# Optimization experiments

Measured on AMD Instinct MI355X. Metric: run time of the kernel, lower is better.

Reference implementation:

```python
import jax, jax.numpy as jnp
import numpy as np

EMBED_DIM = 768
HEADS = 8
HEAD_DIM = 128  # gnn_hidden_dim
OUT_DIM = HEADS * HEAD_DIM  # 1024, concat=True
NEG_SLOPE = 0.2  # PyG GATConv leaky_relu slope


def setup_inputs() -> dict:
    key = jax.random.key(0)
    ks = jax.random.split(key, 12)
    N, E = 10000, 160000
    x = jax.random.normal(ks[0], (N, EMBED_DIM), dtype=jnp.float32)
    edge_index = jax.random.randint(ks[1], (2, E), 0, N, dtype=jnp.int32)
    edge_attr = jax.random.uniform(ks[2], (E, 1), dtype=jnp.float32)
    # GATConv params (single layer, edge_dim=1)
    sc = 1.0 / np.sqrt(EMBED_DIM)
    W = jax.random.normal(ks[3], (EMBED_DIM, OUT_DIM), dtype=jnp.float32) * sc
    att_src = jax.random.normal(ks[4], (HEADS, HEAD_DIM), dtype=jnp.float32) * 0.1
    att_dst = jax.random.normal(ks[5], (HEADS, HEAD_DIM), dtype=jnp.float32) * 0.1
    W_edge = jax.random.normal(ks[6], (1, OUT_DIM), dtype=jnp.float32)
    att_edge = jax.random.normal(ks[7], (HEADS, HEAD_DIM), dtype=jnp.float32) * 0.1
    bias = jnp.zeros((OUT_DIM,), dtype=jnp.float32)
    # final classifier: in = 3*OUT_DIM (global pool + text node + image node)
    clf_W = jax.random.normal(ks[8], (3 * OUT_DIM, 2), dtype=jnp.float32) * (1.0 / np.sqrt(3 * OUT_DIM))
    clf_b = jnp.zeros((2,), dtype=jnp.float32)
    return {
        'x': x, 'edge_index': edge_index, 'edge_attr': edge_attr,
        'text_idx': 0, 'image_idx': 1,
        'W': W, 'att_src': att_src, 'att_dst': att_dst,
        'W_edge': W_edge, 'att_edge': att_edge, 'bias': bias,
        'clf_W': clf_W, 'clf_b': clf_b,
    }


def gat_layer(x, edge_index, edge_attr, W, att_src, att_dst, W_edge, att_edge, bias):
    N = x.shape[0]
    # add self-loops with edge_attr = mean of existing edge_attr (PyG default fill_value='mean')
    loop = jnp.arange(N, dtype=edge_index.dtype)
    ei = jnp.concatenate([edge_index, jnp.stack([loop, loop])], axis=1)
    ea_mean = jnp.mean(edge_attr, axis=0, keepdims=True)
    ea = jnp.concatenate([edge_attr, jnp.broadcast_to(ea_mean, (N, edge_attr.shape[1]))], axis=0)
    src, dst = ei[0], ei[1]
    xs = (x @ W).reshape(N, HEADS, HEAD_DIM)             # [N, H, C]
    a_src = jnp.einsum('nhc,hc->nh', xs, att_src)        # per-node src logits
    a_dst = jnp.einsum('nhc,hc->nh', xs, att_dst)
    e_emb = (ea @ W_edge).reshape(-1, HEADS, HEAD_DIM)   # [Etot, H, C]
    a_edge = jnp.einsum('ehc,hc->eh', e_emb, att_edge)
    alpha = jax.nn.leaky_relu(a_src[src] + a_dst[dst] + a_edge, NEG_SLOPE)  # [Etot, H]
    # softmax over incoming edges of each dst node
    m = jax.ops.segment_max(alpha, dst, num_segments=N)
    ex = jnp.exp(alpha - m[dst])
    denom = jax.ops.segment_sum(ex, dst, num_segments=N)
    w = ex / denom[dst]                                  # normalized attention [Etot, H]
    msg = xs[src] * w[:, :, None]                        # [Etot, H, C]
    out = jax.ops.segment_sum(msg, dst, num_segments=N)  # [N, H, C]
    return out.reshape(N, OUT_DIM) + bias


def reference(x, edge_index, edge_attr, text_idx, image_idx,
              W, att_src, att_dst, W_edge, att_edge, bias, clf_W, clf_b):
    # single GAT layer (num_gat_layers=1 -> no ELU/dropout after, eval mode)
    h = gat_layer(x, edge_index, edge_attr, W, att_src, att_dst, W_edge, att_edge, bias)
    g = jnp.mean(h, axis=0, keepdims=True)               # global_mean_pool, batch=None
    t = h[text_idx][None, :]
    im = h[image_idx][None, :]
    fused = jnp.concatenate([g, t, im], axis=1)          # [1, 3*OUT_DIM]
    logits = fused @ clf_W + clf_b                       # [1, 2]
    return logits
```

## Files before the change

### kernel.cpp

```cpp
#include <hip/hip_runtime.h>

#define NN 10000
#define EE 160000
#define ETOT (EE + NN)
#define EMB 768
#define ODIM 1024
#define NEG 0.2f
#define CAP 56

#define OFF_P      0
#define OFF_Q      12288
#define OFF_EAP    12296
#define OFF_EAACC  12360
#define OFF_CNTD   12364
#define OFF_CNTS   22364
#define ZERO_START 12364
#define ZERO_CNT   20000
#define OFF_A      32368
#define OFF_SAED   192368
#define OFF_DAES   1312368
#define OFF_RDEN   2432368
#define OFF_G      2512368

#define SELF_MARK 3.0e38f

__global__ __launch_bounds__(256) void k1f(
    const float* __restrict__ W, const float* __restrict__ att_src,
    const float* __restrict__ att_dst, const float* __restrict__ W_edge,
    const float* __restrict__ att_edge, const float* __restrict__ edge_attr,
    const float* __restrict__ bias, const float* __restrict__ clf_W,
    const float* __restrict__ clf_b, float* __restrict__ out,
    const int* __restrict__ ei, float* __restrict__ ws) {
  __shared__ float sred[8];
  int b = blockIdx.x;
  if (b < 48) {
    int tid = b * 256 + threadIdx.x;
    int k = tid >> 4, j = tid & 15, h = j & 7;
    const float* att = (j < 8) ? att_src : att_dst;
    const float4* wp = (const float4*)(W + k * ODIM + h * 128);
    const float4* ap = (const float4*)(att + h * 128);
    float acc = 0.f;
    #pragma unroll 8
    for (int c = 0; c < 32; ++c) {
      float4 w4 = wp[c], a4 = ap[c];
      acc += w4.x * a4.x + w4.y * a4.y + w4.z * a4.z + w4.w * a4.w;
    }
    ws[OFF_P + tid] = acc;
  } else if (b == 48) {
    if (threadIdx.x < 8) {
      int h = threadIdx.x;
      float acc = 0.f;
      #pragma unroll 8
      for (int c = 0; c < 128; ++c) acc += W_edge[h * 128 + c] * att_edge[h * 128 + c];
      ws[OFF_Q + h] = acc;
    }
  } else if (b == 49) {
    int t = threadIdx.x;
    float b0 = 0.f, b1 = 0.f;
    for (int i = t; i < 3072; i += 256) {
      float f = bias[i & 1023];
      b0 += f * clf_W[2 * i];
      b1 += f * clf_W[2 * i + 1];
    }
    #pragma unroll
    for (int o = 32; o > 0; o >>= 1) {
      b0 += __shfl_down(b0, o, 64);
      b1 += __shfl_down(b1, o, 64);
    }
    if ((t & 63) == 0) { sred[(t >> 6) * 2] = b0; sred[(t >> 6) * 2 + 1] = b1; }
    __syncthreads();
    if (t == 0) {
      out[0] = clf_b[0] + sred[0] + sred[2] + sred[4] + sred[6];
      out[1] = clf_b[1] + sred[1] + sred[3] + sred[5] + sred[7];
    }
  } else if (b < 74) {
    int t = (b - 50) * 256 + threadIdx.x;
    int k = t >> 3, h = t & 7;
    const float4* wseg = (const float4*)(W + k * ODIM + h * 128);
    float acc[6] = {0.f, 0.f, 0.f, 0.f, 0.f, 0.f};
    for (int c4 = 0; c4 < 32; ++c4) {
      float4 wv = wseg[c4];
      #pragma unroll
      for (int d = 0; d < 3; ++d) {
        const float4* cp = (const float4*)(clf_W + 2 * (1024 * d + h * 128 + c4 * 4));
        float4 q0 = cp[0], q1 = cp[1];
        acc[d * 2 + 0] += wv.x * q0.x + wv.y * q0.z + wv.z * q1.x + wv.w * q1.z;
        acc[d * 2 + 1] += wv.x * q0.y + wv.y * q0.w + wv.z * q1.y + wv.w * q1.w;
      }
    }
    #pragma unroll
    for (int d = 0; d < 3; ++d) {
      ws[OFF_G + d * 12288 + k * 16 + h * 2 + 0] = acc[d * 2 + 0];
      ws[OFF_G + d * 12288 + k * 16 + h * 2 + 1] = acc[d * 2 + 1];
    }
  } else if (b < 138) {
    int bi = b - 74;
    float acc = 0.f;
    for (int i = bi * 256 + threadIdx.x; i < EE; i += 64 * 256) acc += edge_attr[i];
    #pragma unroll
    for (int off = 32; off > 0; off >>= 1) acc += __shfl_down(acc, off, 64);
    if ((threadIdx.x & 63) == 0) sred[threadIdx.x >> 6] = acc;
    __syncthreads();
    if (threadIdx.x == 0)
      ws[OFF_EAP + bi] = sred[0] + sred[1] + sred[2] + sred[3];
  } else {
    int e = (b - 138) * 256 + threadIdx.x;
    if (e >= ETOT) return;
    int src, dst; float ea;
    if (e < EE) { src = ei[e]; dst = ei[EE + e]; ea = edge_attr[e]; }
    else { src = dst = e - EE; ea = SELF_MARK; }
    int* cntd = (int*)(ws + OFF_CNTD);
    int* cnts = (int*)(ws + OFF_CNTS);
    int pd = atomicAdd(&cntd[dst], 1);
    if (pd < CAP) {
      float2 pr; pr.x = __int_as_float(src); pr.y = ea;
      ((float2*)(ws + OFF_SAED))[dst * CAP + pd] = pr;
    }
    int ps = atomicAdd(&cnts[src], 1);
    if (ps < CAP) {
      float2 pr; pr.x = __int_as_float(dst); pr.y = ea;
      ((float2*)(ws + OFF_DAES))[src * CAP + ps] = pr;
    }
  }
}

__global__ __launch_bounds__(256) void kAx(const float* __restrict__ x,
                                           float* __restrict__ ws) {
  __shared__ float smem[12288];
  if (blockIdx.x == 313) {
    if (threadIdx.x < 64) {
      float v = ws[OFF_EAP + threadIdx.x];
      #pragma unroll
      for (int o = 32; o > 0; o >>= 1) v += __shfl_down(v, o, 64);
      if (threadIdx.x == 0) ws[OFF_EAACC] = v;
    }
    return;
  }
  for (int i = threadIdx.x; i < 3072; i += 256)
    ((float4*)smem)[i] = ((const float4*)(ws + OFF_P))[i];
  __syncthreads();
  int nl = threadIdx.x & 31, cg = threadIdx.x >> 5;
  int n = blockIdx.x * 32 + nl;
  float a[16];
  #pragma unroll
  for (int j = 0; j < 16; ++j) a[j] = 0.f;
  if (n < NN) {
    const float4* xr = (const float4*)(x + n * EMB + cg * 96);
    for (int kk = 0; kk < 24; ++kk) {
      float4 xv = xr[kk];
      const float* pr = &smem[(cg * 96 + kk * 4) * 16];
      #pragma unroll
      for (int j = 0; j < 16; ++j) a[j] += xv.x * pr[j];
      #pragma unroll
      for (int j = 0; j < 16; ++j) a[j] += xv.y * pr[16 + j];
      #pragma unroll
      for (int j = 0; j < 16; ++j) a[j] += xv.z * pr[32 + j];
      #pragma unroll
      for (int j = 0; j < 16; ++j) a[j] += xv.w * pr[48 + j];
    }
  }
  __syncthreads();
  #pragma unroll
  for (int j = 0; j < 16; ++j) smem[(cg * 16 + j) * 33 + nl] = a[j];
  __syncthreads();
  for (int w = threadIdx.x; w < 512; w += 256) {
    int rnl = w >> 4, j = w & 15;
    int nn = blockIdx.x * 32 + rnl;
    if (nn < NN) {
      float s = 0.f;
      #pragma unroll
      for (int c2 = 0; c2 < 8; ++c2) s += smem[(c2 * 16 + j) * 33 + rnl];
      ws[OFF_A + nn * 16 + j] = s;
    }
  }
}

__global__ __launch_bounds__(128) void kD(float* __restrict__ ws) {
  int t = blockIdx.x * 128 + threadIdx.x;
  int dst = t >> 3, h = t & 7;
  int deg = ((const int*)(ws + OFF_CNTD))[dst];
  if (deg > CAP) deg = CAP;
  float adh = ws[OFF_A + dst * 16 + 8 + h];
  float qh = ws[OFF_Q + h];
  float mean = ws[OFF_EAACC] * (1.0f / EE);
  const float2* prow = (const float2*)(ws + OFF_SAED) + dst * CAP;
  float den = 0.f;
  #pragma unroll 4
  for (int j = 0; j < deg; ++j) {
    float2 pr = prow[j];
    int srcj = __float_as_int(pr.x);
    float ae = pr.y;
    if (ae > 1e37f) ae = mean;
    float v = ws[OFF_A + srcj * 16 + h] + adh + ae * qh;
    v = (v >= 0.f) ? v : NEG * v;
    den += __expf(v);
  }
  ws[OFF_RDEN + t] = 1.0f / den;
}

__global__ __launch_bounds__(256, 3) void kF(const float* __restrict__ x,
                                             const int* __restrict__ tptr,
                                             const int* __restrict__ iptr,
                                             float* __restrict__ out,
                                             float* __restrict__ ws) {
  __shared__ float smem[12864];
  int t = threadIdx.x;
  float mean = ws[OFF_EAACC] * (1.0f / EE);
  float c0 = 0.f, c1 = 0.f;
  float scale;
  if (blockIdx.x < 625) {
    scale = 1.0f / NN;
    int base = blockIdx.x * 16;
    if (t >= 128) {
      for (int i = t - 128; i < 3072; i += 128)
        ((float4*)smem)[i] = ((const float4*)(ws + OFF_G))[i];
    } else {
      int nl = t >> 3, h = t & 7;
      int n = base + nl;
      int deg = ((const int*)(ws + OFF_CNTS))[n];
      if (deg > CAP) deg = CAP;
      float ash = ws[OFF_A + n * 16 + h];
      float qh = ws[OFF_Q + h];
      const float2* prow = (const float2*)(ws + OFF_DAES) + n * CAP;
      float s = 0.f;
      #pragma unroll 4
      for (int j = 0; j < deg; ++j) {
        float2 pr = prow[j];
        int dd = __float_as_int(pr.x);
        float ae = pr.y;
        if (ae > 1e37f) ae = mean;
        float v = ash + ws[OFF_A + dd * 16 + 8 + h] + ae * qh;
        v = (v >= 0.f) ? v : NEG * v;
        s += __expf(v) * ws[OFF_RDEN + dd * 8 + h];
      }
      smem[12288 + nl * 8 + h] = s;
    }
    __syncthreads();
    int nl = t & 15, cgp = t >> 4;
    int n = base + nl;
    float a[16];
    #pragma unroll
    for (int j = 0; j < 16; ++j) a[j] = 0.f;
    const float4* xr = (const float4*)(x + n * EMB + cgp * 48);
    for (int kk = 0; kk < 12; ++kk) {
      float4 xv = xr[kk];
      const float* pr = &smem[(cgp * 48 + kk * 4) * 16];
      #pragma unroll
      for (int j = 0; j < 16; ++j) a[j] += xv.x * pr[j];
      #pragma unroll
      for (int j = 0; j < 16; ++j) a[j] += xv.y * pr[16 + j];
      #pragma unroll
      for (int j = 0; j < 16; ++j) a[j] += xv.z * pr[32 + j];
      #pragma unroll
      for (int j = 0; j < 16; ++j) a[j] += xv.w * pr[48 + j];
    }
    #pragma unroll
    for (int h = 0; h < 8; ++h) {
      float sv = smem[12288 + nl * 8 + h];
      c0 += sv * a[2 * h];
      c1 += sv * a[2 * h + 1];
    }
  } else {
    scale = 1.0f;
    int d = blockIdx.x - 625;
    int target = (d == 0) ? tptr[0] : iptr[0];
    for (int i = t; i < 3072; i += 256)
      ((float4*)smem)[i] = ((const float4*)(ws + OFF_G + (d + 1) * 12288))[i];
    int deg = ((const int*)(ws + OFF_CNTD))[target];
    if (deg > CAP) deg = CAP;
    for (int idx = t; idx < deg * 8; idx += 256) {
      int j = idx >> 3, h = idx & 7;
      float2 pr = ((const float2*)(ws + OFF_SAED))[target * CAP + j];
      int srcj = __float_as_int(pr.x);
      float ae = pr.y;
      if (ae > 1e37f) ae = mean;
      float v = ws[OFF_A + srcj * 16 + h] + ws[OFF_A + target * 16 + 8 + h]
              + ae * ws[OFF_Q + h];
      v = (v >= 0.f) ? v : NEG * v;
      smem[12288 + j * 8 + h] = __expf(v) * ws[OFF_RDEN + target * 8 + h];
      if (h == 0) ((int*)smem)[12800 + j] = srcj;
    }
    __syncthreads();
    int nl = t & 15, cgp = t >> 4;
    for (int jb = 0; jb * 16 < deg; ++jb) {
      int j = jb * 16 + nl;
      int n = (j < deg) ? ((int*)smem)[12800 + j] : 0;
      float a[16];
      #pragma unroll
      for (int jj = 0; jj < 16; ++jj) a[jj] = 0.f;
      const float4* xr = (const float4*)(x + n * EMB + cgp * 48);
      for (int kk = 0; kk < 12; ++kk) {
        float4 xv = xr[kk];
        const float* pr = &smem[(cgp * 48 + kk * 4) * 16];
        #pragma unroll
        for (int jj = 0; jj < 16; ++jj) a[jj] += xv.x * pr[jj];
        #pragma unroll
        for (int jj = 0; jj < 16; ++jj) a[jj] += xv.y * pr[16 + jj];
        #pragma unroll
        for (int jj = 0; jj < 16; ++jj) a[jj] += xv.z * pr[32 + jj];
        #pragma unroll
        for (int jj = 0; jj < 16; ++jj) a[jj] += xv.w * pr[48 + jj];
      }
      if (j < deg) {
        #pragma unroll
        for (int h = 0; h < 8; ++h) {
          float wv = smem[12288 + j * 8 + h];
          c0 += wv * a[2 * h];
          c1 += wv * a[2 * h + 1];
        }
      }
    }
  }
  #pragma unroll
  for (int o = 32; o > 0; o >>= 1) {
    c0 += __shfl_down(c0, o, 64);
    c1 += __shfl_down(c1, o, 64);
  }
  if ((t & 63) == 0) {
    smem[12856 + (t >> 6) * 2] = c0;
    smem[12857 + (t >> 6) * 2] = c1;
  }
  __syncthreads();
  if (t == 0) {
    float r0 = smem[12856] + smem[12858] + smem[12860] + smem[12862];
    float r1 = smem[12857] + smem[12859] + smem[12861] + smem[12863];
    atomicAdd(&out[0], r0 * scale);
    atomicAdd(&out[1], r1 * scale);
  }
}

extern "C" void kernel_launch(void* const* d_in, const int* in_sizes, int n_in,
                              void* d_out, int out_size, void* d_ws, size_t ws_size,
                              hipStream_t stream) {
  const float* x        = (const float*)d_in[0];
  const int*   ei       = (const int*)d_in[1];
  const float* edge_attr= (const float*)d_in[2];
  const int*   tptr     = (const int*)d_in[3];
  const int*   iptr     = (const int*)d_in[4];
  const float* W        = (const float*)d_in[5];
  const float* att_src  = (const float*)d_in[6];
  const float* att_dst  = (const float*)d_in[7];
  const float* W_edge   = (const float*)d_in[8];
  const float* att_edge = (const float*)d_in[9];
  const float* bias     = (const float*)d_in[10];
  const float* clf_W    = (const float*)d_in[11];
  const float* clf_b    = (const float*)d_in[12];
  float* ws  = (float*)d_ws;
  float* out = (float*)d_out;

  hipMemsetAsync(ws + ZERO_START, 0, ZERO_CNT * sizeof(float), stream);
  k1f<<<803, 256, 0, stream>>>(W, att_src, att_dst, W_edge, att_edge, edge_attr,
                               bias, clf_W, clf_b, out, ei, ws);
  kAx<<<314, 256, 0, stream>>>(x, ws);
  kD<<<625, 128, 0, stream>>>(ws);
  kF<<<627, 256, 0, stream>>>(x, tptr, iptr, out, ws);
}
```

Before: 184.5 us.

## Precompute per-node classifier projections and make global pool edge-parallel

Drops the per-source reverse adjacency (second atomic scatter into DAES) and the x@G projection inside the final kernel. Instead, kAxT computes per-node projections of x onto the pooled classifier table T alongside the attention logits A. The final kernel then runs one thread per edge, combining softmax weights with T[src]. The setup kernel is split in two so the edge scatter no longer shares a launch with the weight precompute. This removes one atomic pass and the gather-heavy per-source loop, at the cost of an extra kernel launch and a second x pass inside kAxT.

```diff
diff --git a/kernel.cpp b/kernel.cpp
--- a/kernel.cpp
+++ b/kernel.cpp
@@ -13,24 +13,22 @@
 #define OFF_EAP    12296
 #define OFF_EAACC  12360
 #define OFF_CNTD   12364
-#define OFF_CNTS   22364
 #define ZERO_START 12364
-#define ZERO_CNT   20000
-#define OFF_A      32368
-#define OFF_SAED   192368
-#define OFF_DAES   1312368
-#define OFF_RDEN   2432368
-#define OFF_G      2512368
+#define ZERO_CNT   10000
+#define OFF_A      22364
+#define OFF_T      182364
+#define OFF_SAED   342364
+#define OFF_RDEN   1462364
+#define OFF_G      1542364
 
 #define SELF_MARK 3.0e38f
 
-__global__ __launch_bounds__(256) void k1f(
+__global__ __launch_bounds__(256) void k1a(
     const float* __restrict__ W, const float* __restrict__ att_src,
     const float* __restrict__ att_dst, const float* __restrict__ W_edge,
-    const float* __restrict__ att_edge, const float* __restrict__ edge_attr,
-    const float* __restrict__ bias, const float* __restrict__ clf_W,
-    const float* __restrict__ clf_b, float* __restrict__ out,
-    const int* __restrict__ ei, float* __restrict__ ws) {
+    const float* __restrict__ att_edge, const float* __restrict__ bias,
+    const float* __restrict__ clf_W, const float* __restrict__ clf_b,
+    float* __restrict__ out, float* __restrict__ ws) {
   __shared__ float sred[8];
   int b = blockIdx.x;
   if (b < 48) {
@@ -73,7 +71,7 @@
       out[0] = clf_b[0] + sred[0] + sred[2] + sred[4] + sred[6];
       out[1] = clf_b[1] + sred[1] + sred[3] + sred[5] + sred[7];
     }
-  } else if (b < 74) {
+  } else {
     int t = (b - 50) * 256 + threadIdx.x;
     int k = t >> 3, h = t & 7;
     const float4* wseg = (const float4*)(W + k * ODIM + h * 128);
@@ -93,39 +91,40 @@
       ws[OFF_G + d * 12288 + k * 16 + h * 2 + 0] = acc[d * 2 + 0];
       ws[OFF_G + d * 12288 + k * 16 + h * 2 + 1] = acc[d * 2 + 1];
     }
-  } else if (b < 138) {
-    int bi = b - 74;
+  }
+}
+
+__global__ __launch_bounds__(256) void k1b(const float* __restrict__ edge_attr,
+                                           const int* __restrict__ ei,
+                                           float* __restrict__ ws) {
+  __shared__ float sred[8];
+  int b = blockIdx.x;
+  if (b < 64) {
     float acc = 0.f;
-    for (int i = bi * 256 + threadIdx.x; i < EE; i += 64 * 256) acc += edge_attr[i];
+    for (int i = b * 256 + threadIdx.x; i < EE; i += 64 * 256) acc += edge_attr[i];
     #pragma unroll
     for (int off = 32; off > 0; off >>= 1) acc += __shfl_down(acc, off, 64);
     if ((threadIdx.x & 63) == 0) sred[threadIdx.x >> 6] = acc;
     __syncthreads();
     if (threadIdx.x == 0)
-      ws[OFF_EAP + bi] = sred[0] + sred[1] + sred[2] + sred[3];
+      ws[OFF_EAP + b] = sred[0] + sred[1] + sred[2] + sred[3];
   } else {
-    int e = (b - 138) * 256 + threadIdx.x;
+    int e = (b - 64) * 256 + threadIdx.x;
     if (e >= ETOT) return;
     int src, dst; float ea;
     if (e < EE) { src = ei[e]; dst = ei[EE + e]; ea = edge_attr[e]; }
     else { src = dst = e - EE; ea = SELF_MARK; }
     int* cntd = (int*)(ws + OFF_CNTD);
-    int* cnts = (int*)(ws + OFF_CNTS);
     int pd = atomicAdd(&cntd[dst], 1);
     if (pd < CAP) {
       float2 pr; pr.x = __int_as_float(src); pr.y = ea;
       ((float2*)(ws + OFF_SAED))[dst * CAP + pd] = pr;
     }
-    int ps = atomicAdd(&cnts[src], 1);
-    if (ps < CAP) {
-      float2 pr; pr.x = __int_as_float(dst); pr.y = ea;
-      ((float2*)(ws + OFF_DAES))[src * CAP + ps] = pr;
-    }
-  }
-}
-
-__global__ __launch_bounds__(256) void kAx(const float* __restrict__ x,
-                                           float* __restrict__ ws) {
+  }
+}
+
+__global__ __launch_bounds__(256) void kAxT(const float* __restrict__ x,
+                                            float* __restrict__ ws) {
   __shared__ float smem[12288];
   if (blockIdx.x == 313) {
     if (threadIdx.x < 64) {
@@ -136,42 +135,48 @@
     }
     return;
   }
-  for (int i = threadIdx.x; i < 3072; i += 256)
-    ((float4*)smem)[i] = ((const float4*)(ws + OFF_P))[i];
-  __syncthreads();
   int nl = threadIdx.x & 31, cg = threadIdx.x >> 5;
   int n = blockIdx.x * 32 + nl;
-  float a[16];
   #pragma unroll
-  for (int j = 0; j < 16; ++j) a[j] = 0.f;
-  if (n < NN) {
-    const float4* xr = (const float4*)(x + n * EMB + cg * 96);
-    for (int kk = 0; kk < 24; ++kk) {
-      float4 xv = xr[kk];
-      const float* pr = &smem[(cg * 96 + kk * 4) * 16];
-      #pragma unroll
-      for (int j = 0; j < 16; ++j) a[j] += xv.x * pr[j];
-      #pragma unroll
-      for (int j = 0; j < 16; ++j) a[j] += xv.y * pr[16 + j];
-      #pragma unroll
-      for (int j = 0; j < 16; ++j) a[j] += xv.z * pr[32 + j];
-      #pragma unroll
-      for (int j = 0; j < 16; ++j) a[j] += xv.w * pr[48 + j];
-    }
-  }
-  __syncthreads();
-  #pragma unroll
-  for (int j = 0; j < 16; ++j) smem[(cg * 16 + j) * 33 + nl] = a[j];
-  __syncthreads();
-  for (int w = threadIdx.x; w < 512; w += 256) {
-    int rnl = w >> 4, j = w & 15;
-    int nn = blockIdx.x * 32 + rnl;
-    if (nn < NN) {
-      float s = 0.f;
-      #pragma unroll
-      for (int c2 = 0; c2 < 8; ++c2) s += smem[(c2 * 16 + j) * 33 + rnl];
-      ws[OFF_A + nn * 16 + j] = s;
-    }
+  for (int pass = 0; pass < 2; ++pass) {
+    const int tbl = (pass == 0) ? OFF_P : OFF_G;
+    const int dstoff = (pass == 0) ? OFF_A : OFF_T;
+    for (int i = threadIdx.x; i < 3072; i += 256)
+      ((float4*)smem)[i] = ((const float4*)(ws + tbl))[i];
+    __syncthreads();
+    float a[16];
+    #pragma unroll
+    for (int j = 0; j < 16; ++j) a[j] = 0.f;
+    if (n < NN) {
+      const float4* xr = (const float4*)(x + n * EMB + cg * 96);
+      for (int kk = 0; kk < 24; ++kk) {
+        float4 xv = xr[kk];
+        const float* pr = &smem[(cg * 96 + kk * 4) * 16];
+        #pragma unroll
+        for (int j = 0; j < 16; ++j) a[j] += xv.x * pr[j];
+        #pragma unroll
+        for (int j = 0; j < 16; ++j) a[j] += xv.y * pr[16 + j];
+        #pragma unroll
+        for (int j = 0; j < 16; ++j) a[j] += xv.z * pr[32 + j];
+        #pragma unroll
+        for (int j = 0; j < 16; ++j) a[j] += xv.w * pr[48 + j];
+      }
+    }
+    __syncthreads();
+    #pragma unroll
+    for (int j = 0; j < 16; ++j) smem[(cg * 16 + j) * 33 + nl] = a[j];
+    __syncthreads();
+    for (int w = threadIdx.x; w < 512; w += 256) {
+      int rnl = w >> 4, j = w & 15;
+      int nn = blockIdx.x * 32 + rnl;
+      if (nn < NN) {
+        float s = 0.f;
+        #pragma unroll
+        for (int c2 = 0; c2 < 8; ++c2) s += smem[(c2 * 16 + j) * 33 + rnl];
+        ws[dstoff + nn * 16 + j] = s;
+      }
+    }
+    __syncthreads();
   }
 }
 
@@ -198,71 +203,49 @@
   ws[OFF_RDEN + t] = 1.0f / den;
 }
 
-__global__ __launch_bounds__(256, 3) void kF(const float* __restrict__ x,
-                                             const int* __restrict__ tptr,
-                                             const int* __restrict__ iptr,
-                                             float* __restrict__ out,
-                                             float* __restrict__ ws) {
+__global__ __launch_bounds__(256, 3) void kFin(const float* __restrict__ x,
+                                               const int* __restrict__ ei,
+                                               const float* __restrict__ edge_attr,
+                                               const int* __restrict__ tptr,
+                                               const int* __restrict__ iptr,
+                                               float* __restrict__ out,
+                                               float* __restrict__ ws) {
   __shared__ float smem[12864];
   int t = threadIdx.x;
   float mean = ws[OFF_EAACC] * (1.0f / EE);
   float c0 = 0.f, c1 = 0.f;
   float scale;
-  if (blockIdx.x < 625) {
+  if (blockIdx.x < 665) {
     scale = 1.0f / NN;
-    int base = blockIdx.x * 16;
-    if (t >= 128) {
-      for (int i = t - 128; i < 3072; i += 128)
-        ((float4*)smem)[i] = ((const float4*)(ws + OFF_G))[i];
-    } else {
-      int nl = t >> 3, h = t & 7;
-      int n = base + nl;
-      int deg = ((const int*)(ws + OFF_CNTS))[n];
-      if (deg > CAP) deg = CAP;
-      float ash = ws[OFF_A + n * 16 + h];
-      float qh = ws[OFF_Q + h];
-      const float2* prow = (const float2*)(ws + OFF_DAES) + n * CAP;
-      float s = 0.f;
-      #pragma unroll 4
-      for (int j = 0; j < deg; ++j) {
-        float2 pr = prow[j];
-        int dd = __float_as_int(pr.x);
-        float ae = pr.y;
-        if (ae > 1e37f) ae = mean;
-        float v = ash + ws[OFF_A + dd * 16 + 8 + h] + ae * qh;
+    int e = blockIdx.x * 256 + t;
+    if (e < ETOT) {
+      int src, dst; float ea;
+      if (e < EE) { src = ei[e]; dst = ei[EE + e]; ea = edge_attr[e]; }
+      else { src = dst = e - EE; ea = mean; }
+      const float4* as4 = (const float4*)(ws + OFF_A + src * 16);
+      const float4* ad4 = (const float4*)(ws + OFF_A + dst * 16 + 8);
+      const float4* rd4 = (const float4*)(ws + OFF_RDEN + dst * 8);
+      const float4* t4  = (const float4*)(ws + OFF_T + src * 16);
+      float4 s0 = as4[0], s1 = as4[1], d0 = ad4[0], d1 = ad4[1];
+      float4 r0 = rd4[0], r1 = rd4[1];
+      float4 t0 = t4[0], t1 = t4[1], t2 = t4[2], t3 = t4[3];
+      float asr[8] = {s0.x, s0.y, s0.z, s0.w, s1.x, s1.y, s1.z, s1.w};
+      float ads[8] = {d0.x, d0.y, d0.z, d0.w, d1.x, d1.y, d1.z, d1.w};
+      float rdn[8] = {r0.x, r0.y, r0.z, r0.w, r1.x, r1.y, r1.z, r1.w};
+      float tt[16] = {t0.x, t0.y, t0.z, t0.w, t1.x, t1.y, t1.z, t1.w,
+                      t2.x, t2.y, t2.z, t2.w, t3.x, t3.y, t3.z, t3.w};
+      #pragma unroll
+      for (int h = 0; h < 8; ++h) {
+        float v = asr[h] + ads[h] + ea * ws[OFF_Q + h];
         v = (v >= 0.f) ? v : NEG * v;
-        s += __expf(v) * ws[OFF_RDEN + dd * 8 + h];
-      }
-      smem[12288 + nl * 8 + h] = s;
-    }
-    __syncthreads();
-    int nl = t & 15, cgp = t >> 4;
-    int n = base + nl;
-    float a[16];
-    #pragma unroll
-    for (int j = 0; j < 16; ++j) a[j] = 0.f;
-    const float4* xr = (const float4*)(x + n * EMB + cgp * 48);
-    for (int kk = 0; kk < 12; ++kk) {
-      float4 xv = xr[kk];
-      const float* pr = &smem[(cgp * 48 + kk * 4) * 16];
-      #pragma unroll
-      for (int j = 0; j < 16; ++j) a[j] += xv.x * pr[j];
-      #pragma unroll
-      for (int j = 0; j < 16; ++j) a[j] += xv.y * pr[16 + j];
-      #pragma unroll
-      for (int j = 0; j < 16; ++j) a[j] += xv.z * pr[32 + j];
-      #pragma unroll
-      for (int j = 0; j < 16; ++j) a[j] += xv.w * pr[48 + j];
-    }
-    #pragma unroll
-    for (int h = 0; h < 8; ++h) {
-      float sv = smem[12288 + nl * 8 + h];
-      c0 += sv * a[2 * h];
-      c1 += sv * a[2 * h + 1];
+        float w = __expf(v) * rdn[h];
+        c0 += w * tt[2 * h];
+        c1 += w * tt[2 * h + 1];
+      }
     }
   } else {
     scale = 1.0f;
-    int d = blockIdx.x - 625;
+    int d = blockIdx.x - 665;
     int target = (d == 0) ? tptr[0] : iptr[0];
     for (int i = t; i < 3072; i += 256)
       ((float4*)smem)[i] = ((const float4*)(ws + OFF_G + (d + 1) * 12288))[i];
@@ -349,9 +332,10 @@
   float* out = (float*)d_out;
 
   hipMemsetAsync(ws + ZERO_START, 0, ZERO_CNT * sizeof(float), stream);
-  k1f<<<803, 256, 0, stream>>>(W, att_src, att_dst, W_edge, att_edge, edge_attr,
-                               bias, clf_W, clf_b, out, ei, ws);
-  kAx<<<314, 256, 0, stream>>>(x, ws);
+  k1a<<<74, 256, 0, stream>>>(W, att_src, att_dst, W_edge, att_edge,
+                              bias, clf_W, clf_b, out, ws);
+  k1b<<<729, 256, 0, stream>>>(edge_attr, ei, ws);
+  kAxT<<<314, 256, 0, stream>>>(x, ws);
   kD<<<625, 128, 0, stream>>>(ws);
-  kF<<<627, 256, 0, stream>>>(x, tptr, iptr, out, ws);
-}
+  kFin<<<667, 256, 0, stream>>>(x, ei, edge_attr, tptr, iptr, out, ws);
+}
```

After: 193.2 us. 4.7% more time.
